# Kernel tuning notes

Hardware: AMD Instinct MI355X
Metric: run time of the kernel (lower is better)

## Reference

```python
import jax, jax.numpy as jnp
import numpy as np
from jax.scipy.special import gammaln

N_L, N_Q, D_IN, D_CTX, H, MAX_AGENT = 256, 65536, 384, 192, 64, 6
STD2 = 0.1
VAR2 = STD2 * STD2
LOG_VAR2 = float(np.log(VAR2))
TEMP = 1.0


def _linear_init(k, out_dim, in_dim):
    k1, k2 = jax.random.split(k)
    s = 1.0 / np.sqrt(in_dim)
    w = jax.random.uniform(k1, (out_dim, in_dim), minval=-s, maxval=s, dtype=jnp.float32)
    b = jax.random.uniform(k2, (out_dim,), minval=-s, maxval=s, dtype=jnp.float32)
    return w, b


def setup_inputs() -> dict:
    key = jax.random.key(0)
    ks = jax.random.split(key, 12)
    fc1_w, fc1_b = _linear_init(ks[0], H, D_IN)
    fc21_w, fc21_b = _linear_init(ks[1], H, H)
    fc22_w, fc22_b = _linear_init(ks[2], H, H)
    fc3_w, fc3_b = _linear_init(ks[3], H, H)
    fc4_w, fc4_b = _linear_init(ks[4], D_IN, H)
    ctx_w, ctx_b = _linear_init(ks[5], H, D_CTX)
    llms = jax.random.normal(ks[6], (N_L, D_IN), dtype=jnp.float32)
    contexts = jax.random.normal(ks[7], (N_Q, D_CTX), dtype=jnp.float32)
    agent_num_int = jax.random.randint(ks[8], (N_Q, 1), 1, MAX_AGENT + 1, dtype=jnp.int32)
    agent_num_float = agent_num_int.astype(jnp.float32)
    noise_eps = jax.random.normal(ks[9], (N_L, H), dtype=jnp.float32)   # VAE reparameterize eps
    rand_u = jax.random.uniform(ks[10], (MAX_AGENT, N_Q, 1), dtype=jnp.float32)  # per-step uniforms
    return dict(llms=llms, contexts=contexts, agent_num_int=agent_num_int,
                agent_num_float=agent_num_float,
                fc1_w=fc1_w, fc1_b=fc1_b, fc21_w=fc21_w, fc21_b=fc21_b,
                fc22_w=fc22_w, fc22_b=fc22_b, fc3_w=fc3_w, fc3_b=fc3_b,
                fc4_w=fc4_w, fc4_b=fc4_b, ctx_w=ctx_w, ctx_b=ctx_b,
                noise_eps=noise_eps, rand_u=rand_u)


def _l2norm(x):
    n = jnp.sqrt(jnp.sum(x * x, axis=1, keepdims=True))
    return x / jnp.maximum(n, 1e-12)


def reference(llms, contexts, agent_num_int, agent_num_float,
              fc1_w, fc1_b, fc21_w, fc21_b, fc22_w, fc22_b,
              fc3_w, fc3_b, fc4_w, fc4_b, ctx_w, ctx_b, noise_eps, rand_u):
    # ---- VAE encode / reparameterize / decode ----
    h = jax.nn.relu(llms @ fc1_w.T + fc1_b)
    mu = h @ fc21_w.T + fc21_b
    log_var = h @ fc22_w.T + fc22_b
    std = jnp.exp(0.5 * log_var) * STD2
    z = mu + noise_eps * std
    h2 = jax.nn.relu(z @ fc3_w.T + fc3_b)
    x_hat = h2 @ fc4_w.T + fc4_b
    mse = jnp.mean((x_hat - llms) ** 2)
    kld = -0.5 * jnp.mean(1.0 - LOG_VAR2 + log_var - (mu ** 2 + jnp.exp(log_var)) / VAR2)
    vae_loss = mse + kld

    # ---- embeddings and routing scores ----
    llm_emb = _l2norm(z)                                   # [N_l, H]
    ctx_emb = _l2norm(contexts @ ctx_w.T + ctx_b)          # [N_q, H]
    scores = jax.nn.softmax((ctx_emb @ llm_emb.T) / TEMP, axis=1)  # [N_q, N_l]
    scores_cumsum = jnp.cumsum(scores, axis=1)

    # ---- vectorized max_agent-step categorical sampling ----
    # sel[i, q] = first llm where cumsum > u (inverse-CDF sampling), for step i
    sel = jnp.argmax(scores_cumsum[None, :, :] > rand_u, axis=2)          # [A, N_q]
    steps = jnp.arange(1, rand_u.shape[0] + 1, dtype=agent_num_int.dtype)
    mask = (agent_num_int[None, :, 0] >= steps[:, None]).astype(scores.dtype)  # [A, N_q]
    rows = jnp.broadcast_to(jnp.arange(scores.shape[0])[None, :], sel.shape)
    selected_llm = jnp.zeros_like(scores).at[rows, sel].add(mask)          # [N_q, N_l]

    log_probs = (gammaln(agent_num_float + 1.0)
                 - jnp.sum(gammaln(selected_llm + 1.0), axis=1, keepdims=True)
                 + jnp.sum(selected_llm * jnp.log(scores), axis=1, keepdims=True))
    return selected_llm, log_probs, vae_loss
```

## Files before the change

### kernel.cpp

```cpp
#include <hip/hip_runtime.h>
#include <hip/hip_bf16.h>

#define N_L 256
#define N_Q 65536
#define D_IN 384
#define D_CTX 192
#define HDIM 64
#define MAXA 6

__device__ __forceinline__ void fma4(float& acc, const float4& w, const float4& v) {
    acc = fmaf(w.x, v.x, acc);
    acc = fmaf(w.y, v.y, acc);
    acc = fmaf(w.z, v.z, acc);
    acc = fmaf(w.w, v.w, acc);
}

__device__ __forceinline__ float lgfact(int n) {
    return (n <= 1) ? 0.0f :
           (n == 2) ? 0.6931471805599453f :
           (n == 3) ? 1.7917594692280550f :
           (n == 4) ? 3.1780538303479458f :
           (n == 5) ? 4.7874917427820460f :
                      6.5792512120101010f;
}

__device__ __forceinline__ float rfl_f(float x) {
    return __int_as_float(__builtin_amdgcn_readfirstlane(__float_as_int(x)));
}

__global__ __launch_bounds__(64) void vae_kernel(
    const float* __restrict__ llms, const float* __restrict__ ctx_w,
    const float* __restrict__ fc1_w, const float* __restrict__ fc1_b,
    const float* __restrict__ fc21_w, const float* __restrict__ fc21_b,
    const float* __restrict__ fc22_w, const float* __restrict__ fc22_b,
    const float* __restrict__ fc3_w, const float* __restrict__ fc3_b,
    const float* __restrict__ fc4_w, const float* __restrict__ fc4_b,
    const float* __restrict__ eps,
    float* __restrict__ ctx_wT, float* __restrict__ embT,
    float* __restrict__ mse_row, float* __restrict__ kld_row)
{
    __shared__ __align__(16) float xs[D_IN];
    __shared__ __align__(16) float hs[HDIM];
    __shared__ __align__(16) float zs[HDIM];
    __shared__ __align__(16) float h2s[HDIM];
    const int r = blockIdx.x;
    const int j = threadIdx.x;

    {
        int t = r * 64 + j;
        if (t < D_CTX * HDIM) ctx_wT[t] = ctx_w[(t & 63) * D_CTX + (t >> 6)];
    }

    for (int k = j; k < D_IN; k += 64) xs[k] = llms[r * D_IN + k];
    __syncthreads();

    float acc = fc1_b[j];
    {
        const float4* wr = (const float4*)(fc1_w + (size_t)j * D_IN);
        const float4* xr = (const float4*)xs;
        #pragma unroll 8
        for (int k4 = 0; k4 < D_IN / 4; ++k4) { fma4(acc, wr[k4], xr[k4]); }
    }
    float h = fmaxf(acc, 0.0f);
    hs[j] = h;
    __syncthreads();

    float mu = fc21_b[j], lv = fc22_b[j];
    {
        const float4* w1 = (const float4*)(fc21_w + (size_t)j * HDIM);
        const float4* w2 = (const float4*)(fc22_w + (size_t)j * HDIM);
        const float4* hr = (const float4*)hs;
        #pragma unroll
        for (int k4 = 0; k4 < HDIM / 4; ++k4) {
            float4 hh = hr[k4];
            fma4(mu, w1[k4], hh);
            fma4(lv, w2[k4], hh);
        }
    }
    float stdv = expf(0.5f * lv) * 0.1f;
    float z = fmaf(eps[r * HDIM + j], stdv, mu);

    float elv = expf(lv);
    float kt = (1.0f - (-4.60517018598809136f)) + lv - (mu * mu + elv) / 0.01f;
    float ks = kt;
    #pragma unroll
    for (int o = 32; o; o >>= 1) ks += __shfl_xor(ks, o);

    float zsq = z * z;
    #pragma unroll
    for (int o = 32; o; o >>= 1) zsq += __shfl_xor(zsq, o);
    float nrm = fmaxf(sqrtf(zsq), 1e-12f);
    embT[j * N_L + r] = z / nrm;
    zs[j] = z;
    __syncthreads();

    float a3 = fc3_b[j];
    {
        const float4* w3 = (const float4*)(fc3_w + (size_t)j * HDIM);
        const float4* zr = (const float4*)zs;
        #pragma unroll
        for (int k4 = 0; k4 < HDIM / 4; ++k4) { fma4(a3, w3[k4], zr[k4]); }
    }
    float h2 = fmaxf(a3, 0.0f);
    h2s[j] = h2;
    __syncthreads();

    float ms = 0.0f;
    const float4* h2r = (const float4*)h2s;
    #pragma unroll
    for (int m = 0; m < 6; ++m) {
        int o = j + 64 * m;
        float a4 = fc4_b[o];
        const float4* w4 = (const float4*)(fc4_w + (size_t)o * HDIM);
        #pragma unroll
        for (int k4 = 0; k4 < HDIM / 4; ++k4) { fma4(a4, w4[k4], h2r[k4]); }
        float d = a4 - xs[o];
        ms = fmaf(d, d, ms);
    }
    #pragma unroll
    for (int o = 32; o; o >>= 1) ms += __shfl_xor(ms, o);
    if (j == 0) { mse_row[r] = ms; kld_row[r] = ks; }
}

__global__ __launch_bounds__(256) void route_kernel(
    const float* __restrict__ contexts, const float* __restrict__ ctx_wT, const float* __restrict__ ctx_b,
    const float* __restrict__ embT, const int* __restrict__ agent_num, const float* __restrict__ rand_u,
    const float* __restrict__ mse_row, const float* __restrict__ kld_row,
    float* __restrict__ out_sel, float* __restrict__ out_lp, float* __restrict__ out_loss)
{
    __shared__ __align__(16) float elds[4][8 * HDIM];

    const int tid = threadIdx.x;
    const int lane = tid & 63;
    const int widx = tid >> 6;
    const int l0 = lane << 2;

    const int g = blockIdx.x * 4 + widx;
    const int q0 = __builtin_amdgcn_readfirstlane(g << 3);
    float* ew = elds[widx];

    if (g == 0) {
        int rr = lane * 4;
        float ms = mse_row[rr] + mse_row[rr + 1] + mse_row[rr + 2] + mse_row[rr + 3];
        float ks = kld_row[rr] + kld_row[rr + 1] + kld_row[rr + 2] + kld_row[rr + 3];
        #pragma unroll
        for (int o = 32; o; o >>= 1) { ms += __shfl_xor(ms, o); ks += __shfl_xor(ks, o); }
        if (lane == 0) out_loss[0] = ms / 98304.0f - 0.5f * (ks / 16384.0f);
    }

    const float bj = ctx_b[lane];
    float e[8];
    #pragma unroll
    for (int q = 0; q < 8; ++q) e[q] = bj;
    #pragma unroll 2
    for (int k4 = 0; k4 < D_CTX / 4; ++k4) {
        float w0 = ctx_wT[(k4 * 4 + 0) * HDIM + lane];
        float w1 = ctx_wT[(k4 * 4 + 1) * HDIM + lane];
        float w2 = ctx_wT[(k4 * 4 + 2) * HDIM + lane];
        float w3 = ctx_wT[(k4 * 4 + 3) * HDIM + lane];
        #pragma unroll
        for (int q = 0; q < 8; ++q) {
            float4 xv = *(const float4*)(contexts + (size_t)(q0 + q) * D_CTX + k4 * 4);
            e[q] = fmaf(w0, xv.x, e[q]);
            e[q] = fmaf(w1, xv.y, e[q]);
            e[q] = fmaf(w2, xv.z, e[q]);
            e[q] = fmaf(w3, xv.w, e[q]);
        }
    }
    {
        float s[8];
        #pragma unroll
        for (int q = 0; q < 8; ++q) s[q] = e[q] * e[q];
        #pragma unroll
        for (int o = 32; o; o >>= 1)
            #pragma unroll
            for (int q = 0; q < 8; ++q) s[q] += __shfl_xor(s[q], o);
        #pragma unroll
        for (int q = 0; q < 8; ++q) {
            e[q] *= 1.0f / fmaxf(sqrtf(s[q]), 1e-12f);
            ew[q * HDIM + lane] = e[q];
        }
    }

    float4 P[8];
    #pragma unroll
    for (int q = 0; q < 8; ++q) P[q] = make_float4(0.f, 0.f, 0.f, 0.f);

    #pragma unroll 2
    for (int j4 = 0; j4 < HDIM / 4; ++j4) {
        float4 M0 = *(const float4*)(embT + (size_t)(j4 * 4 + 0) * N_L + l0);
        float4 M1 = *(const float4*)(embT + (size_t)(j4 * 4 + 1) * N_L + l0);
        float4 M2 = *(const float4*)(embT + (size_t)(j4 * 4 + 2) * N_L + l0);
        float4 M3 = *(const float4*)(embT + (size_t)(j4 * 4 + 3) * N_L + l0);
        #pragma unroll
        for (int q = 0; q < 8; ++q) {
            float4 ev = *(const float4*)(ew + q * HDIM + j4 * 4);
            P[q].x = fmaf(M0.x, ev.x, P[q].x); P[q].x = fmaf(M1.x, ev.y, P[q].x);
            P[q].x = fmaf(M2.x, ev.z, P[q].x); P[q].x = fmaf(M3.x, ev.w, P[q].x);
            P[q].y = fmaf(M0.y, ev.x, P[q].y); P[q].y = fmaf(M1.y, ev.y, P[q].y);
            P[q].y = fmaf(M2.y, ev.z, P[q].y); P[q].y = fmaf(M3.y, ev.w, P[q].y);
            P[q].z = fmaf(M0.z, ev.x, P[q].z); P[q].z = fmaf(M1.z, ev.y, P[q].z);
            P[q].z = fmaf(M2.z, ev.z, P[q].z); P[q].z = fmaf(M3.z, ev.w, P[q].z);
            P[q].w = fmaf(M0.w, ev.x, P[q].w); P[q].w = fmaf(M1.w, ev.y, P[q].w);
            P[q].w = fmaf(M2.w, ev.z, P[q].w); P[q].w = fmaf(M3.w, ev.w, P[q].w);
        }
    }

    int Aq[8];
    #pragma unroll
    for (int q = 0; q < 8; ++q)
        Aq[q] = __builtin_amdgcn_readfirstlane(agent_num[q0 + q]);
    float uu[MAXA][8];
    #pragma unroll
    for (int i = 0; i < MAXA; ++i)
        #pragma unroll
        for (int q = 0; q < 8; ++q)
            uu[i][q] = rfl_f(rand_u[i * N_Q + q0 + q]);

    {
        float m[8], s[8];
        #pragma unroll
        for (int k = 0; k < 8; ++k) m[k] = fmaxf(fmaxf(P[k].x, P[k].y), fmaxf(P[k].z, P[k].w));
        #pragma unroll
        for (int o = 32; o; o >>= 1)
            #pragma unroll
            for (int k = 0; k < 8; ++k) m[k] = fmaxf(m[k], __shfl_xor(m[k], o));
        #pragma unroll
        for (int k = 0; k < 8; ++k) {
            P[k].x = expf(P[k].x - m[k]); P[k].y = expf(P[k].y - m[k]);
            P[k].z = expf(P[k].z - m[k]); P[k].w = expf(P[k].w - m[k]);
            s[k] = P[k].x + P[k].y + P[k].z + P[k].w;
        }
        #pragma unroll
        for (int o = 32; o; o >>= 1)
            #pragma unroll
            for (int k = 0; k < 8; ++k) s[k] += __shfl_xor(s[k], o);
        #pragma unroll
        for (int k = 0; k < 8; ++k) {
            float inv = 1.0f / s[k];
            P[k].x *= inv; P[k].y *= inv; P[k].z *= inv; P[k].w *= inv;
        }
    }

    float c0[8], c1[8], c2[8], c3[8];
    {
        float p3[8], t[8];
        #pragma unroll
        for (int k = 0; k < 8; ++k) {
            c0[k] = P[k].x; c1[k] = c0[k] + P[k].y; c2[k] = c1[k] + P[k].z; p3[k] = c2[k] + P[k].w;
            t[k] = p3[k];
        }
        #pragma unroll
        for (int o = 1; o < 64; o <<= 1)
            #pragma unroll
            for (int k = 0; k < 8; ++k) { float v = __shfl_up(t[k], o); if (lane >= o) t[k] += v; }
        #pragma unroll
        for (int k = 0; k < 8; ++k) {
            float base = t[k] - p3[k];
            c0[k] += base; c1[k] += base; c2[k] += base; c3[k] = p3[k] + base;
        }
    }

    unsigned nib[8] = {0, 0, 0, 0, 0, 0, 0, 0};
    #pragma unroll
    for (int i = 0; i < MAXA; ++i) {
        #pragma unroll
        for (int k = 0; k < 8; ++k) {
            if (i < Aq[k]) {
                float u = uu[i][k];
                unsigned long long b0 = __ballot(c0[k] <= u);
                unsigned long long b1 = __ballot(c1[k] <= u);
                unsigned long long b2 = __ballot(c2[k] <= u);
                unsigned long long b3 = __ballot(c3[k] <= u);
                int loc = __popcll(b0) + __popcll(b1) + __popcll(b2) + __popcll(b3);
                int sel = (loc >= N_L) ? 0 : loc;
                unsigned d = (unsigned)(sel - l0);
                if (d < 4u) nib[k] += 1u << (4 * d);
            }
        }
    }

    float term[8];
    #pragma unroll
    for (int k = 0; k < 8; ++k) {
        int n0 = nib[k] & 15, n1 = (nib[k] >> 4) & 15, n2 = (nib[k] >> 8) & 15, n3 = (nib[k] >> 12) & 15;
        float4 rowv = make_float4((float)n0, (float)n1, (float)n2, (float)n3);
        *(((float4*)(out_sel + (size_t)(q0 + k) * N_L)) + lane) = rowv;
        float tm = 0.0f;
        if (n0) tm += (float)n0 * logf(P[k].x) - lgfact(n0);
        if (n1) tm += (float)n1 * logf(P[k].y) - lgfact(n1);
        if (n2) tm += (float)n2 * logf(P[k].z) - lgfact(n2);
        if (n3) tm += (float)n3 * logf(P[k].w) - lgfact(n3);
        term[k] = tm;
    }
    #pragma unroll
    for (int o = 32; o; o >>= 1)
        #pragma unroll
        for (int k = 0; k < 8; ++k) term[k] += __shfl_xor(term[k], o);

    if (lane < 8) {
        float rr = term[0];
        int Aa = Aq[0];
        #pragma unroll
        for (int k = 1; k < 8; ++k) {
            if (lane == k) { rr = term[k]; Aa = Aq[k]; }
        }
        out_lp[q0 + lane] = lgfact(Aa) + rr;
    }
}

extern "C" void kernel_launch(void* const* d_in, const int* in_sizes, int n_in,
                              void* d_out, int out_size, void* d_ws, size_t ws_size,
                              hipStream_t stream) {
    const float* llms      = (const float*)d_in[0];
    const float* contexts  = (const float*)d_in[1];
    const int*   agent_i   = (const int*)  d_in[2];
    const float* fc1_w  = (const float*)d_in[4];  const float* fc1_b  = (const float*)d_in[5];
    const float* fc21_w = (const float*)d_in[6];  const float* fc21_b = (const float*)d_in[7];
    const float* fc22_w = (const float*)d_in[8];  const float* fc22_b = (const float*)d_in[9];
    const float* fc3_w  = (const float*)d_in[10]; const float* fc3_b  = (const float*)d_in[11];
    const float* fc4_w  = (const float*)d_in[12]; const float* fc4_b  = (const float*)d_in[13];
    const float* ctx_w  = (const float*)d_in[14]; const float* ctx_b  = (const float*)d_in[15];
    const float* noise  = (const float*)d_in[16]; const float* rand_u = (const float*)d_in[17];

    float* out      = (float*)d_out;
    float* out_sel  = out;
    float* out_lp   = out + (size_t)N_Q * N_L;
    float* out_loss = out_lp + N_Q;

    float* ctx_wT   = (float*)d_ws;
    float* embT     = ctx_wT + D_CTX * HDIM;
    float* mse_row  = embT + HDIM * N_L;
    float* kld_row  = mse_row + N_L;

    vae_kernel<<<N_L, 64, 0, stream>>>(llms, ctx_w, fc1_w, fc1_b, fc21_w, fc21_b, fc22_w, fc22_b,
                                       fc3_w, fc3_b, fc4_w, fc4_b, noise,
                                       ctx_wT, embT, mse_row, kld_row);
    route_kernel<<<2048, 256, 0, stream>>>(contexts, ctx_wT, ctx_b, embT, agent_i, rand_u,
                                           mse_row, kld_row, out_sel, out_lp, out_loss);
}
```

Measured before the change: 254.7 us.

## Stage contexts and rand_u in LDS, pack ctx weights as float4

Each wave now loads its 8 context rows with coalesced float4 loads into LDS, along with the 48 uniform samples. The projection loop reads contexts from LDS, so it no longer issues scalar/broadcast global loads per k-step. The ctx weight is repacked so that each lane fetches one float4 per k4 instead of four separate floats, and the agent-count loads are moved earlier. LDS per block grows from 8KB to about 25KB, which may reduce occupancy, and the context staging area is later reused for the embeddings.

```diff
diff --git a/kernel.cpp b/kernel.cpp
--- a/kernel.cpp
+++ b/kernel.cpp
@@ -22,10 +22,6 @@
            (n == 4) ? 3.1780538303479458f :
            (n == 5) ? 4.7874917427820460f :
                       6.5792512120101010f;
-}
-
-__device__ __forceinline__ float rfl_f(float x) {
-    return __int_as_float(__builtin_amdgcn_readfirstlane(__float_as_int(x)));
 }
 
 __global__ __launch_bounds__(64) void vae_kernel(
@@ -36,7 +32,7 @@
     const float* __restrict__ fc3_w, const float* __restrict__ fc3_b,
     const float* __restrict__ fc4_w, const float* __restrict__ fc4_b,
     const float* __restrict__ eps,
-    float* __restrict__ ctx_wT, float* __restrict__ embT,
+    float* __restrict__ ctx_wP, float* __restrict__ embT,
     float* __restrict__ mse_row, float* __restrict__ kld_row)
 {
     __shared__ __align__(16) float xs[D_IN];
@@ -47,8 +43,12 @@
     const int j = threadIdx.x;
 
     {
-        int t = r * 64 + j;
-        if (t < D_CTX * HDIM) ctx_wT[t] = ctx_w[(t & 63) * D_CTX + (t >> 6)];
+        int f = r * 64 + j;
+        if (f < D_CTX * HDIM) {
+            int p = f >> 2, rr = f & 3;
+            int jc = p & 63, k4 = p >> 6;
+            ctx_wP[f] = ctx_w[jc * D_CTX + k4 * 4 + rr];
+        }
     }
 
     for (int k = j; k < D_IN; k += 64) xs[k] = llms[r * D_IN + k];
@@ -123,12 +123,12 @@
 }
 
 __global__ __launch_bounds__(256) void route_kernel(
-    const float* __restrict__ contexts, const float* __restrict__ ctx_wT, const float* __restrict__ ctx_b,
+    const float* __restrict__ contexts, const float* __restrict__ ctx_wP, const float* __restrict__ ctx_b,
     const float* __restrict__ embT, const int* __restrict__ agent_num, const float* __restrict__ rand_u,
     const float* __restrict__ mse_row, const float* __restrict__ kld_row,
     float* __restrict__ out_sel, float* __restrict__ out_lp, float* __restrict__ out_loss)
 {
-    __shared__ __align__(16) float elds[4][8 * HDIM];
+    __shared__ __align__(16) float lds[4][1600];
 
     const int tid = threadIdx.x;
     const int lane = tid & 63;
@@ -137,7 +137,19 @@
 
     const int g = blockIdx.x * 4 + widx;
     const int q0 = __builtin_amdgcn_readfirstlane(g << 3);
-    float* ew = elds[widx];
+    float* myl = lds[widx];
+
+    {
+        float4* xls = (float4*)myl;
+        const float4* cbase = (const float4*)contexts + (size_t)q0 * (D_CTX / 4);
+        #pragma unroll
+        for (int it = 0; it < 6; ++it) {
+            int f = lane + it * 64;
+            xls[f] = cbase[f];
+        }
+        if (lane < 48)
+            myl[1536 + lane] = rand_u[(lane >> 3) * N_Q + q0 + (lane & 7)];
+    }
 
     if (g == 0) {
         int rr = lane * 4;
@@ -148,23 +160,29 @@
         if (lane == 0) out_loss[0] = ms / 98304.0f - 0.5f * (ks / 16384.0f);
     }
 
+    int Aq[8];
+    #pragma unroll
+    for (int q = 0; q < 8; ++q)
+        Aq[q] = __builtin_amdgcn_readfirstlane(agent_num[q0 + q]);
+
     const float bj = ctx_b[lane];
     float e[8];
     #pragma unroll
     for (int q = 0; q < 8; ++q) e[q] = bj;
-    #pragma unroll 2
-    for (int k4 = 0; k4 < D_CTX / 4; ++k4) {
-        float w0 = ctx_wT[(k4 * 4 + 0) * HDIM + lane];
-        float w1 = ctx_wT[(k4 * 4 + 1) * HDIM + lane];
-        float w2 = ctx_wT[(k4 * 4 + 2) * HDIM + lane];
-        float w3 = ctx_wT[(k4 * 4 + 3) * HDIM + lane];
-        #pragma unroll
-        for (int q = 0; q < 8; ++q) {
-            float4 xv = *(const float4*)(contexts + (size_t)(q0 + q) * D_CTX + k4 * 4);
-            e[q] = fmaf(w0, xv.x, e[q]);
-            e[q] = fmaf(w1, xv.y, e[q]);
-            e[q] = fmaf(w2, xv.z, e[q]);
-            e[q] = fmaf(w3, xv.w, e[q]);
+    {
+        const float4* wp = (const float4*)ctx_wP;
+        const float4* xls = (const float4*)myl;
+        #pragma unroll 2
+        for (int k4 = 0; k4 < D_CTX / 4; ++k4) {
+            float4 w = wp[k4 * HDIM + lane];
+            #pragma unroll
+            for (int q = 0; q < 8; ++q) {
+                float4 xv = xls[q * 48 + k4];
+                e[q] = fmaf(w.x, xv.x, e[q]);
+                e[q] = fmaf(w.y, xv.y, e[q]);
+                e[q] = fmaf(w.z, xv.z, e[q]);
+                e[q] = fmaf(w.w, xv.w, e[q]);
+            }
         }
     }
     {
@@ -178,7 +196,7 @@
         #pragma unroll
         for (int q = 0; q < 8; ++q) {
             e[q] *= 1.0f / fmaxf(sqrtf(s[q]), 1e-12f);
-            ew[q * HDIM + lane] = e[q];
+            myl[q * HDIM + lane] = e[q];
         }
     }
 
@@ -194,7 +212,7 @@
         float4 M3 = *(const float4*)(embT + (size_t)(j4 * 4 + 3) * N_L + l0);
         #pragma unroll
         for (int q = 0; q < 8; ++q) {
-            float4 ev = *(const float4*)(ew + q * HDIM + j4 * 4);
+            float4 ev = *(const float4*)(myl + q * HDIM + j4 * 4);
             P[q].x = fmaf(M0.x, ev.x, P[q].x); P[q].x = fmaf(M1.x, ev.y, P[q].x);
             P[q].x = fmaf(M2.x, ev.z, P[q].x); P[q].x = fmaf(M3.x, ev.w, P[q].x);
             P[q].y = fmaf(M0.y, ev.x, P[q].y); P[q].y = fmaf(M1.y, ev.y, P[q].y);
@@ -206,17 +224,6 @@
         }
     }
 
-    int Aq[8];
-    #pragma unroll
-    for (int q = 0; q < 8; ++q)
-        Aq[q] = __builtin_amdgcn_readfirstlane(agent_num[q0 + q]);
-    float uu[MAXA][8];
-    #pragma unroll
-    for (int i = 0; i < MAXA; ++i)
-        #pragma unroll
-        for (int q = 0; q < 8; ++q)
-            uu[i][q] = rfl_f(rand_u[i * N_Q + q0 + q]);
-
     {
         float m[8], s[8];
         #pragma unroll
@@ -267,7 +274,7 @@
         #pragma unroll
         for (int k = 0; k < 8; ++k) {
             if (i < Aq[k]) {
-                float u = uu[i][k];
+                float u = myl[1536 + i * 8 + k];
                 unsigned long long b0 = __ballot(c0[k] <= u);
                 unsigned long long b1 = __ballot(c1[k] <= u);
                 unsigned long long b2 = __ballot(c2[k] <= u);
@@ -328,14 +335,14 @@
     float* out_lp   = out + (size_t)N_Q * N_L;
     float* out_loss = out_lp + N_Q;
 
-    float* ctx_wT   = (float*)d_ws;
-    float* embT     = ctx_wT + D_CTX * HDIM;
+    float* ctx_wP   = (float*)d_ws;
+    float* embT     = ctx_wP + D_CTX * HDIM;
     float* mse_row  = embT + HDIM * N_L;
     float* kld_row  = mse_row + N_L;
 
     vae_kernel<<<N_L, 64, 0, stream>>>(llms, ctx_w, fc1_w, fc1_b, fc21_w, fc21_b, fc22_w, fc22_b,
                                        fc3_w, fc3_b, fc4_w, fc4_b, noise,
-                                       ctx_wT, embT, mse_row, kld_row);
-    route_kernel<<<2048, 256, 0, stream>>>(contexts, ctx_wT, ctx_b, embT, agent_i, rand_u,
+                                       ctx_wP, embT, mse_row, kld_row);
+    route_kernel<<<2048, 256, 0, stream>>>(contexts, ctx_wP, ctx_b, embT, agent_i, rand_u,
                                            mse_row, kld_row, out_sel, out_lp, out_loss);
 }
```

Measured after the change: 228.6 us, median of 2. 10.2% less time.
